# Performance work log

Measured on AMD Instinct MI355X. Metric: run time of the kernel, lower is better.

The kernel has to match this reference:

```python
import jax, jax.numpy as jnp
import numpy as np

N_NODES = 50000


def _gcn_norm(edge_index, num_nodes):
    # PyG GCNConv default: add self-loops, symmetric normalization D^-1/2 A D^-1/2
    row, col = edge_index[0], edge_index[1]
    loop = jnp.arange(num_nodes, dtype=edge_index.dtype)
    row = jnp.concatenate([row, loop])
    col = jnp.concatenate([col, loop])
    deg = jax.ops.segment_sum(jnp.ones_like(col, dtype=jnp.float32), col,
                              num_segments=num_nodes)
    deg_inv_sqrt = jnp.where(deg > 0, jax.lax.rsqrt(deg), 0.0)
    norm = deg_inv_sqrt[row] * deg_inv_sqrt[col]  # [E + N]
    return row, col, norm


def _gcn_conv(x, row, col, norm, W, b):
    h = x @ W                                   # [N, out]
    msg = h[row] * norm[:, None]                # gather + scale, [E+N, out]
    out = jax.ops.segment_sum(msg, col, num_segments=x.shape[0])  # scatter-add
    return out + b


def setup_inputs() -> dict:
    key = jax.random.key(0)
    k_x, k_e, k_w1, k_w2 = jax.random.split(key, 4)
    n, e, d = N_NODES, 800000, 64
    x = jax.random.normal(k_x, (n, d), dtype=jnp.float32)
    edge_index = jax.random.randint(k_e, (2, e), 0, n, dtype=jnp.int64)
    # Glorot init like PyG's Linear inside GCNConv (bias separate, zero-init here as randn-small)
    s1 = (6.0 / (d + d)) ** 0.5
    W1 = jax.random.uniform(k_w1, (d, d), jnp.float32, -s1, s1)
    W2 = jax.random.uniform(k_w2, (d, d), jnp.float32, -s1, s1)
    b1 = jnp.zeros((d,), jnp.float32)
    b2 = jnp.zeros((d,), jnp.float32)
    return {"x": x, "edge_index": edge_index, "W1": W1, "b1": b1, "W2": W2, "b2": b2}


def reference(x, edge_index, W1, b1, W2, b2):
    row, col, norm = _gcn_norm(edge_index, x.shape[0])
    h = _gcn_conv(x, row, col, norm, W1, b1)   # layer 1: in -> out
    h = _gcn_conv(h, row, col, norm, W2, b2)   # layer 2: out -> out
    return h
```

## Files before the change

### kernel.cpp

```cpp
#include <hip/hip_runtime.h>
#include <hip/hip_fp16.h>

#define DD 64
#define BSH 6
#define BNODES 64
#define NSUB 16
#define SCAP 128
#define BCAP 1536

__global__ __launch_bounds__(256) void k_zero(int4* __restrict__ p, int n4) {
    int i = blockIdx.x * 256 + threadIdx.x;
    if (i < n4) p[i] = make_int4(0, 0, 0, 0);
}

__global__ __launch_bounds__(256) void k_fill3(const int* __restrict__ rowi,
                                               const int* __restrict__ coli,
                                               int* __restrict__ cur,
                                               unsigned int* __restrict__ pk, int E) {
    int i = blockIdx.x * 256 + threadIdx.x;
    if (i < E) {
        int c = coli[i];
        int idx = (c >> BSH) * NSUB + (blockIdx.x & (NSUB - 1));
        int p = atomicAdd(&cur[idx * 16], 1);
        if (p < SCAP)
            pk[(size_t)idx * SCAP + p] =
                (unsigned int)rowi[i] | ((unsigned int)(c & (BNODES - 1)) << 16);
    }
}

__global__ __launch_bounds__(256) void k_bsort(const int* __restrict__ cur,
                                               const unsigned int* __restrict__ pk,
                                               int* __restrict__ off_s,
                                               int* __restrict__ off_e,
                                               float* __restrict__ dis,
                                               int* __restrict__ srt, int n) {
    __shared__ unsigned int stage[NSUB * SCAP];
    __shared__ int cnt[BNODES];
    __shared__ int cbase[BNODES];
    __shared__ int sb[NSUB + 1];
    int t = threadIdx.x;
    int b = blockIdx.x;

    if (t < BNODES) cnt[t] = 0;
    if (t < NSUB) {
        int v = cur[(b * NSUB + t) * 16];
        if (v > SCAP) v = SCAP;
        int x = v;
#pragma unroll
        for (int d = 1; d < NSUB; d <<= 1) {
            int u = __shfl_up(x, d, NSUB);
            if ((t & (NSUB - 1)) >= d) x += u;
        }
        sb[t + 1] = x;
        if (t == 0) sb[0] = 0;
    }
    __syncthreads();
    int tot = sb[NSUB];

#pragma unroll
    for (int s = 0; s < NSUB; ++s) {
        int c0 = sb[s], len = sb[s + 1] - c0;
        const unsigned int* src = pk + ((size_t)b * NSUB + s) * SCAP;
        for (int i = t; i < len; i += 256) stage[c0 + i] = src[i];
    }
    __syncthreads();

    for (int i = t; i < tot; i += 256) atomicAdd(&cnt[stage[i] >> 16], 1);
    __syncthreads();

    if (t < BNODES) {
        int v = cnt[t], x = v;
#pragma unroll
        for (int d = 1; d < 64; d <<= 1) {
            int u = __shfl_up(x, d);
            if (t >= d) x += u;
        }
        int excl = x - v;
        cbase[t] = excl;
        int c = b * BNODES + t;
        if (c < n) {
            off_s[c] = b * BCAP + excl;
            off_e[c] = b * BCAP + excl + v;
            dis[c] = rsqrtf((float)(v + 1));
        }
    }
    __syncthreads();

    int sbeg = b * BCAP;
    for (int i = t; i < tot; i += 256) {
        unsigned int k = stage[i];
        int pos = atomicAdd(&cbase[k >> 16], 1);
        srt[sbeg + pos] = (int)(k & 0xFFFFu);
    }
}

__global__ __launch_bounds__(64) void k_mm(const float* __restrict__ X,
                                           const float* __restrict__ W,
                                           const float* __restrict__ dis,
                                           __half* __restrict__ H, int n) {
    int lane  = threadIdx.x;
    int tile  = blockIdx.x >> 1;
    int jbase = (blockIdx.x & 1) * 32;
    int r     = tile * 64 + lane;
    int rc    = min(r, n - 1);

    const float4* X4 = (const float4*)X;
    float acc[32];
#pragma unroll
    for (int j = 0; j < 32; ++j) acc[j] = 0.f;

#pragma unroll 1
    for (int kc = 0; kc < 16; ++kc) {
        float4 xv = X4[(size_t)rc * 16 + kc];
        const float* W0 = W + (kc * 4) * 64 + jbase;
#pragma unroll
        for (int u = 0; u < 4; ++u) {
            float xk = (u == 0) ? xv.x : (u == 1) ? xv.y : (u == 2) ? xv.z : xv.w;
            const float* Wk = W0 + u * 64;
#pragma unroll
            for (int j = 0; j < 32; ++j)
                acc[j] = fmaf(xk, Wk[j], acc[j]);
        }
    }
    if (r < n) {
        float d = dis[r];
        __half2 hh[16];
#pragma unroll
        for (int q = 0; q < 16; ++q)
            hh[q] = __floats2half2_rn(acc[2 * q] * d, acc[2 * q + 1] * d);
        uint4* dst = (uint4*)(H + (size_t)r * DD + jbase);
        const uint4* src = (const uint4*)hh;
#pragma unroll
        for (int q = 0; q < 4; ++q) dst[q] = src[q];
    }
}

__global__ __launch_bounds__(256) void k_agg(const int* __restrict__ off_s,
                                             const int* __restrict__ off_e,
                                             const int* __restrict__ srt,
                                             const float* __restrict__ dis,
                                             const __half* __restrict__ hs,
                                             const float* __restrict__ bias,
                                             float* __restrict__ out, int n, int totW) {
    int lane = threadIdx.x & 63;
    int j    = lane & 31;
    int hsel = lane >> 5;
    int wid  = __builtin_amdgcn_readfirstlane(blockIdx.x * 4 + (threadIdx.x >> 6));
    const __half2* hs2 = (const __half2*)hs;

    for (int c = wid; c < n; c += totW) {
        int s = __builtin_amdgcn_readfirstlane(off_s[c]);
        int e = __builtin_amdgcn_readfirstlane(off_e[c]);

        float ax = 0.f, ay = 0.f;
        if (hsel == 0) {
            float2 f = __half22float2(hs2[(size_t)c * 32 + j]);
            ax = f.x; ay = f.y;
        }
        int p = s;
        for (; p + 8 <= e; p += 8) {
            int r0 = srt[p + 0], r1 = srt[p + 1], r2 = srt[p + 2], r3 = srt[p + 3];
            int r4 = srt[p + 4], r5 = srt[p + 5], r6 = srt[p + 6], r7 = srt[p + 7];
            int ra = hsel ? r1 : r0;
            int rb = hsel ? r3 : r2;
            int rg = hsel ? r5 : r4;
            int rd = hsel ? r7 : r6;
            float2 f0 = __half22float2(hs2[(size_t)ra * 32 + j]);
            float2 f1 = __half22float2(hs2[(size_t)rb * 32 + j]);
            float2 f2 = __half22float2(hs2[(size_t)rg * 32 + j]);
            float2 f3 = __half22float2(hs2[(size_t)rd * 32 + j]);
            ax += (f0.x + f1.x) + (f2.x + f3.x);
            ay += (f0.y + f1.y) + (f2.y + f3.y);
        }
        for (; p + 2 <= e; p += 2) {
            int r0 = srt[p], r1 = srt[p + 1];
            int ra = hsel ? r1 : r0;
            float2 f = __half22float2(hs2[(size_t)ra * 32 + j]);
            ax += f.x; ay += f.y;
        }
        if (p < e && hsel == 0) {
            float2 f = __half22float2(hs2[(size_t)srt[p] * 32 + j]);
            ax += f.x; ay += f.y;
        }
        ax += __shfl_xor(ax, 32);
        ay += __shfl_xor(ay, 32);
        if (hsel == 0) {
            float d = dis[c];
            float2 bb = ((const float2*)bias)[j];
            ((float2*)out)[(size_t)c * 32 + j] = make_float2(bb.x + d * ax, bb.y + d * ay);
        }
    }
}

extern "C" void kernel_launch(void* const* d_in, const int* in_sizes, int n_in,
                              void* d_out, int out_size, void* d_ws, size_t ws_size,
                              hipStream_t stream) {
    const float* x  = (const float*)d_in[0];
    const int*   ei = (const int*)d_in[1];
    const float* W1 = (const float*)d_in[2];
    const float* b1 = (const float*)d_in[3];
    const float* W2 = (const float*)d_in[4];
    const float* b2 = (const float*)d_in[5];
    float* out = (float*)d_out;

    int n = in_sizes[0] / DD;
    int E = in_sizes[1] / 2;
    const int* rowi = ei;
    const int* coli = ei + E;
    int nb = (n + BNODES - 1) / BNODES;
    int M  = nb * NSUB;

    char* ws = (char*)d_ws;
    int*          cur   = (int*)ws;
    int*          off_s = (int*)(ws + (size_t)1024 * 1024);
    int*          off_e = (int*)(ws + (size_t)1280 * 1024);
    float*        dis   = (float*)(ws + (size_t)1536 * 1024);
    unsigned int* pk    = (unsigned int*)(ws + (size_t)2048 * 1024);
    int*          srt   = (int*)(ws + (size_t)8704 * 1024);
    __half*       hs    = (__half*)(ws + (size_t)14336 * 1024);
    float*        o1    = out;

    int n4    = M * 4;
    int nb_z  = (n4 + 255) / 256;
    int nb_e  = (E + 255) / 256;
    int nb_mm = ((n + 63) / 64) * 2;
    int nb_ag = 2048;
    int totW  = nb_ag * 4;

    k_zero <<<nb_z, 256, 0, stream>>>((int4*)cur, n4);
    k_fill3<<<nb_e, 256, 0, stream>>>(rowi, coli, cur, pk, E);
    k_bsort<<<nb, 256, 0, stream>>>(cur, pk, off_s, off_e, dis, srt, n);

    k_mm <<<nb_mm, 64, 0, stream>>>(x, W1, dis, hs, n);
    k_agg<<<nb_ag, 256, 0, stream>>>(off_s, off_e, srt, dis, hs, b1, o1, n, totW);

    k_mm <<<nb_mm, 64, 0, stream>>>(o1, W2, dis, hs, n);
    k_agg<<<nb_ag, 256, 0, stream>>>(off_s, off_e, srt, dis, hs, b2, out, n, totW);
}
```

Before: 132.8 us.

## Fuse layer-1 matmul into bucket sort, fp16 intermediate, one-node-per-wave aggregation

The bucket-sort kernel now also loads the X tile into shared memory and computes the first X@W1 product, scaled by the in-block degree normalisation. That removes a separate launch and the dependency on a global dis write. The layer-1 aggregation writes its output in half precision, and the second matmul reads half input, which halves intermediate traffic but adds rounding error. The sub-bucket count changes from 16 to 8 with a larger capacity, and the aggregation switches from a grid-stride loop to one wave per node.

```diff
diff --git a/kernel.cpp b/kernel.cpp
--- a/kernel.cpp
+++ b/kernel.cpp
@@ -4,8 +4,8 @@
 #define DD 64
 #define BSH 6
 #define BNODES 64
-#define NSUB 16
-#define SCAP 128
+#define NSUB 8
+#define SCAP 256
 #define BCAP 1536
 
 __global__ __launch_bounds__(256) void k_zero(int4* __restrict__ p, int n4) {
@@ -28,18 +28,24 @@
     }
 }
 
-__global__ __launch_bounds__(256) void k_bsort(const int* __restrict__ cur,
-                                               const unsigned int* __restrict__ pk,
-                                               int* __restrict__ off_s,
-                                               int* __restrict__ off_e,
-                                               float* __restrict__ dis,
-                                               int* __restrict__ srt, int n) {
+__global__ __launch_bounds__(256) void k_bsortmm(const int* __restrict__ cur,
+                                                 const unsigned int* __restrict__ pk,
+                                                 int* __restrict__ off_s,
+                                                 int* __restrict__ off_e,
+                                                 float* __restrict__ dis,
+                                                 int* __restrict__ srt,
+                                                 const float* __restrict__ X,
+                                                 const float* __restrict__ W,
+                                                 __half* __restrict__ H, int n) {
     __shared__ unsigned int stage[NSUB * SCAP];
+    __shared__ float xs[BNODES * 65];
     __shared__ int cnt[BNODES];
     __shared__ int cbase[BNODES];
     __shared__ int sb[NSUB + 1];
-    int t = threadIdx.x;
-    int b = blockIdx.x;
+    __shared__ float sdis[BNODES];
+    const int t = threadIdx.x;
+    const int b = blockIdx.x;
+    const int c0 = b * BNODES;
 
     if (t < BNODES) cnt[t] = 0;
     if (t < NSUB) {
@@ -59,9 +65,20 @@
 
 #pragma unroll
     for (int s = 0; s < NSUB; ++s) {
-        int c0 = sb[s], len = sb[s + 1] - c0;
+        int q0 = sb[s], len = sb[s + 1] - q0;
         const unsigned int* src = pk + ((size_t)b * NSUB + s) * SCAP;
-        for (int i = t; i < len; i += 256) stage[c0 + i] = src[i];
+        for (int i = t; i < len; i += 256) stage[q0 + i] = src[i];
+    }
+    {
+        const float4* X4 = (const float4*)X;
+        for (int idx = t; idx < BNODES * 16; idx += 256) {
+            int row = idx >> 4, q = idx & 15, c = c0 + row;
+            float4 v = make_float4(0.f, 0.f, 0.f, 0.f);
+            if (c < n) v = X4[(size_t)c * 16 + q];
+            int base = row * 65 + q * 4;
+            xs[base + 0] = v.x; xs[base + 1] = v.y;
+            xs[base + 2] = v.z; xs[base + 3] = v.w;
+        }
     }
     __syncthreads();
 
@@ -77,11 +94,13 @@
         }
         int excl = x - v;
         cbase[t] = excl;
-        int c = b * BNODES + t;
+        float dv = rsqrtf((float)(v + 1));
+        sdis[t] = dv;
+        int c = c0 + t;
         if (c < n) {
             off_s[c] = b * BCAP + excl;
             off_e[c] = b * BCAP + excl + v;
-            dis[c] = rsqrtf((float)(v + 1));
+            dis[c] = dv;
         }
     }
     __syncthreads();
@@ -92,34 +111,69 @@
         int pos = atomicAdd(&cbase[k >> 16], 1);
         srt[sbeg + pos] = (int)(k & 0xFFFFu);
     }
-}
-
-__global__ __launch_bounds__(64) void k_mm(const float* __restrict__ X,
-                                           const float* __restrict__ W,
-                                           const float* __restrict__ dis,
-                                           __half* __restrict__ H, int n) {
+    __syncthreads();
+
+    const int lane  = t & 63;
+    const int jbase = __builtin_amdgcn_readfirstlane((t >> 6) * 16);
+    float acc[16];
+#pragma unroll
+    for (int j = 0; j < 16; ++j) acc[j] = 0.f;
+#pragma unroll 1
+    for (int kc = 0; kc < 16; ++kc) {
+#pragma unroll
+        for (int u = 0; u < 4; ++u) {
+            float sk = xs[lane * 65 + kc * 4 + u];
+            const float* Wk = W + (kc * 4 + u) * 64 + jbase;
+#pragma unroll
+            for (int j = 0; j < 16; ++j)
+                acc[j] = fmaf(sk, Wk[j], acc[j]);
+        }
+    }
+    int c = c0 + lane;
+    if (c < n) {
+        float d = sdis[lane];
+        __half2 hh[8];
+#pragma unroll
+        for (int q = 0; q < 8; ++q)
+            hh[q] = __floats2half2_rn(acc[2 * q] * d, acc[2 * q + 1] * d);
+        uint4* dst = (uint4*)(H + (size_t)c * DD + jbase);
+        const uint4* src = (const uint4*)hh;
+        dst[0] = src[0];
+        dst[1] = src[1];
+    }
+}
+
+__global__ __launch_bounds__(64) void k_mm_h(const __half* __restrict__ Xh,
+                                             const float* __restrict__ W,
+                                             const float* __restrict__ dis,
+                                             __half* __restrict__ H, int n) {
     int lane  = threadIdx.x;
     int tile  = blockIdx.x >> 1;
     int jbase = (blockIdx.x & 1) * 32;
     int r     = tile * 64 + lane;
     int rc    = min(r, n - 1);
 
-    const float4* X4 = (const float4*)X;
+    const uint4* X8 = (const uint4*)Xh;
     float acc[32];
 #pragma unroll
     for (int j = 0; j < 32; ++j) acc[j] = 0.f;
 
 #pragma unroll 1
-    for (int kc = 0; kc < 16; ++kc) {
-        float4 xv = X4[(size_t)rc * 16 + kc];
-        const float* W0 = W + (kc * 4) * 64 + jbase;
-#pragma unroll
-        for (int u = 0; u < 4; ++u) {
-            float xk = (u == 0) ? xv.x : (u == 1) ? xv.y : (u == 2) ? xv.z : xv.w;
-            const float* Wk = W0 + u * 64;
+    for (int kc = 0; kc < 8; ++kc) {
+        uint4 hv = X8[(size_t)rc * 8 + kc];
+        float xk[8];
+        const __half2* hp = (const __half2*)&hv;
+#pragma unroll
+        for (int q = 0; q < 4; ++q) {
+            float2 f = __half22float2(hp[q]);
+            xk[2 * q] = f.x; xk[2 * q + 1] = f.y;
+        }
+#pragma unroll
+        for (int u = 0; u < 8; ++u) {
+            const float* Wk = W + (kc * 8 + u) * 64 + jbase;
 #pragma unroll
             for (int j = 0; j < 32; ++j)
-                acc[j] = fmaf(xk, Wk[j], acc[j]);
+                acc[j] = fmaf(xk[u], Wk[j], acc[j]);
         }
     }
     if (r < n) {
@@ -135,60 +189,67 @@
     }
 }
 
+template<int HOUT>
 __global__ __launch_bounds__(256) void k_agg(const int* __restrict__ off_s,
                                              const int* __restrict__ off_e,
                                              const int* __restrict__ srt,
                                              const float* __restrict__ dis,
                                              const __half* __restrict__ hs,
                                              const float* __restrict__ bias,
-                                             float* __restrict__ out, int n, int totW) {
+                                             float* __restrict__ outf,
+                                             __half* __restrict__ outh, int n) {
     int lane = threadIdx.x & 63;
     int j    = lane & 31;
     int hsel = lane >> 5;
-    int wid  = __builtin_amdgcn_readfirstlane(blockIdx.x * 4 + (threadIdx.x >> 6));
+    int c = __builtin_amdgcn_readfirstlane(blockIdx.x * 4 + (threadIdx.x >> 6));
+    if (c >= n) return;
+
+    int s = __builtin_amdgcn_readfirstlane(off_s[c]);
+    int e = __builtin_amdgcn_readfirstlane(off_e[c]);
+
     const __half2* hs2 = (const __half2*)hs;
 
-    for (int c = wid; c < n; c += totW) {
-        int s = __builtin_amdgcn_readfirstlane(off_s[c]);
-        int e = __builtin_amdgcn_readfirstlane(off_e[c]);
-
-        float ax = 0.f, ay = 0.f;
-        if (hsel == 0) {
-            float2 f = __half22float2(hs2[(size_t)c * 32 + j]);
-            ax = f.x; ay = f.y;
-        }
-        int p = s;
-        for (; p + 8 <= e; p += 8) {
-            int r0 = srt[p + 0], r1 = srt[p + 1], r2 = srt[p + 2], r3 = srt[p + 3];
-            int r4 = srt[p + 4], r5 = srt[p + 5], r6 = srt[p + 6], r7 = srt[p + 7];
-            int ra = hsel ? r1 : r0;
-            int rb = hsel ? r3 : r2;
-            int rg = hsel ? r5 : r4;
-            int rd = hsel ? r7 : r6;
-            float2 f0 = __half22float2(hs2[(size_t)ra * 32 + j]);
-            float2 f1 = __half22float2(hs2[(size_t)rb * 32 + j]);
-            float2 f2 = __half22float2(hs2[(size_t)rg * 32 + j]);
-            float2 f3 = __half22float2(hs2[(size_t)rd * 32 + j]);
-            ax += (f0.x + f1.x) + (f2.x + f3.x);
-            ay += (f0.y + f1.y) + (f2.y + f3.y);
-        }
-        for (; p + 2 <= e; p += 2) {
-            int r0 = srt[p], r1 = srt[p + 1];
-            int ra = hsel ? r1 : r0;
-            float2 f = __half22float2(hs2[(size_t)ra * 32 + j]);
-            ax += f.x; ay += f.y;
-        }
-        if (p < e && hsel == 0) {
-            float2 f = __half22float2(hs2[(size_t)srt[p] * 32 + j]);
-            ax += f.x; ay += f.y;
-        }
-        ax += __shfl_xor(ax, 32);
-        ay += __shfl_xor(ay, 32);
-        if (hsel == 0) {
-            float d = dis[c];
-            float2 bb = ((const float2*)bias)[j];
-            ((float2*)out)[(size_t)c * 32 + j] = make_float2(bb.x + d * ax, bb.y + d * ay);
-        }
+    float ax = 0.f, ay = 0.f;
+    if (hsel == 0) {
+        float2 f = __half22float2(hs2[(size_t)c * 32 + j]);
+        ax = f.x; ay = f.y;
+    }
+    int p = s;
+    for (; p + 8 <= e; p += 8) {
+        int r0 = srt[p + 0], r1 = srt[p + 1], r2 = srt[p + 2], r3 = srt[p + 3];
+        int r4 = srt[p + 4], r5 = srt[p + 5], r6 = srt[p + 6], r7 = srt[p + 7];
+        int ra = hsel ? r1 : r0;
+        int rb = hsel ? r3 : r2;
+        int rg = hsel ? r5 : r4;
+        int rd = hsel ? r7 : r6;
+        float2 f0 = __half22float2(hs2[(size_t)ra * 32 + j]);
+        float2 f1 = __half22float2(hs2[(size_t)rb * 32 + j]);
+        float2 f2 = __half22float2(hs2[(size_t)rg * 32 + j]);
+        float2 f3 = __half22float2(hs2[(size_t)rd * 32 + j]);
+        ax += (f0.x + f1.x) + (f2.x + f3.x);
+        ay += (f0.y + f1.y) + (f2.y + f3.y);
+    }
+    for (; p + 2 <= e; p += 2) {
+        int r0 = srt[p], r1 = srt[p + 1];
+        int ra = hsel ? r1 : r0;
+        float2 f = __half22float2(hs2[(size_t)ra * 32 + j]);
+        ax += f.x; ay += f.y;
+    }
+    if (p < e && hsel == 0) {
+        float2 f = __half22float2(hs2[(size_t)srt[p] * 32 + j]);
+        ax += f.x; ay += f.y;
+    }
+    ax += __shfl_xor(ax, 32);
+    ay += __shfl_xor(ay, 32);
+    if (hsel == 0) {
+        float d = dis[c];
+        float2 bb = ((const float2*)bias)[j];
+        float ox = bb.x + d * ax;
+        float oy = bb.y + d * ay;
+        if (HOUT)
+            ((__half2*)outh)[(size_t)c * 32 + j] = __floats2half2_rn(ox, oy);
+        else
+            ((float2*)outf)[(size_t)c * 32 + j] = make_float2(ox, oy);
     }
 }
 
@@ -216,24 +277,24 @@
     int*          off_e = (int*)(ws + (size_t)1280 * 1024);
     float*        dis   = (float*)(ws + (size_t)1536 * 1024);
     unsigned int* pk    = (unsigned int*)(ws + (size_t)2048 * 1024);
-    int*          srt   = (int*)(ws + (size_t)8704 * 1024);
+    int*          srt   = (int*)(ws + (size_t)9216 * 1024);
     __half*       hs    = (__half*)(ws + (size_t)14336 * 1024);
-    float*        o1    = out;
+    __half*       o1h   = (__half*)(ws + (size_t)21504 * 1024);
 
     int n4    = M * 4;
     int nb_z  = (n4 + 255) / 256;
     int nb_e  = (E + 255) / 256;
     int nb_mm = ((n + 63) / 64) * 2;
-    int nb_ag = 2048;
-    int totW  = nb_ag * 4;
-
-    k_zero <<<nb_z, 256, 0, stream>>>((int4*)cur, n4);
-    k_fill3<<<nb_e, 256, 0, stream>>>(rowi, coli, cur, pk, E);
-    k_bsort<<<nb, 256, 0, stream>>>(cur, pk, off_s, off_e, dis, srt, n);
-
-    k_mm <<<nb_mm, 64, 0, stream>>>(x, W1, dis, hs, n);
-    k_agg<<<nb_ag, 256, 0, stream>>>(off_s, off_e, srt, dis, hs, b1, o1, n, totW);
-
-    k_mm <<<nb_mm, 64, 0, stream>>>(o1, W2, dis, hs, n);
-    k_agg<<<nb_ag, 256, 0, stream>>>(off_s, off_e, srt, dis, hs, b2, out, n, totW);
-}
+    int nb_ag = (n + 3) / 4;
+
+    k_zero   <<<nb_z, 256, 0, stream>>>((int4*)cur, n4);
+    k_fill3  <<<nb_e, 256, 0, stream>>>(rowi, coli, cur, pk, E);
+    k_bsortmm<<<nb, 256, 0, stream>>>(cur, pk, off_s, off_e, dis, srt, x, W1, hs, n);
+
+    k_agg<1><<<nb_ag, 256, 0, stream>>>(off_s, off_e, srt, dis, hs, b1,
+                                        (float*)nullptr, o1h, n);
+
+    k_mm_h  <<<nb_mm, 64, 0, stream>>>(o1h, W2, dis, hs, n);
+    k_agg<0><<<nb_ag, 256, 0, stream>>>(off_s, off_e, srt, dis, hs, b2,
+                                        out, (__half*)nullptr, n);
+}
```

Measured after the change: 129.6 us. -2.4%, faster.
